# Performance work log

Measured on AMD Instinct MI355X. Metric: run time of the kernel, lower is better.

The kernel has to match this reference:

```python
import jax, jax.numpy as jnp
import numpy as np

BS = 512          # number of nodes (batch)
EMBED = 256       # embed_dim
NHEAD = 8
HDIM = EMBED // NHEAD
E = BS * BS       # fully-connected intra-batch graph


def _xavier(key, shape):
    lim = float(np.sqrt(6.0 / (shape[0] + shape[1])))
    return jax.random.uniform(key, shape, jnp.float32, -lim, lim)


def setup_inputs() -> dict:
    key = jax.random.key(0)
    ks = jax.random.split(key, 6)
    feats = jax.random.normal(ks[0], (BS, EMBED), jnp.float32)
    # edges sorted by destination c, exactly BS edges per destination
    dst = jnp.repeat(jnp.arange(BS), BS)   # c
    src = jnp.tile(jnp.arange(BS), BS)     # r
    edge_index = jnp.stack([src, dst], axis=1).astype(jnp.int32)  # [E, 2], cols (r, c)
    edge_attr = jnp.zeros((E, 1), jnp.float32)  # unused by forward
    return {
        "feats": feats,
        "edge_index": edge_index,
        "edge_attr": edge_attr,
        "Wq": _xavier(ks[1], (EMBED, EMBED)), "bq": jnp.zeros((EMBED,), jnp.float32),
        "Wk": _xavier(ks[2], (EMBED, EMBED)), "bk": jnp.zeros((EMBED,), jnp.float32),
        "Wv": _xavier(ks[3], (EMBED, EMBED)), "bv": jnp.zeros((EMBED,), jnp.float32),
        "Wo": _xavier(ks[4], (EMBED, EMBED)), "bo": jnp.zeros((EMBED,), jnp.float32),
    }


def reference(feats, edge_index, edge_attr, Wq, bq, Wk, bk, Wv, bv, Wo, bo):
    bs = feats.shape[0]
    scale = 1.0 / np.sqrt(HDIM)
    # QKV projections (torch Linear: x @ W.T + b), split heads -> [h, n, d]
    q = (feats @ Wq.T + bq).reshape(bs, NHEAD, HDIM).transpose(1, 0, 2)
    k = (feats @ Wk.T + bk).reshape(bs, NHEAD, HDIM).transpose(1, 0, 2)
    v = (feats @ Wv.T + bv).reshape(bs, NHEAD, HDIM).transpose(1, 0, 2)
    r, c = edge_index[:, 0], edge_index[:, 1]
    qe = q[:, c, :]   # [h, E, d] query of destination node
    ke = k[:, r, :]   # [h, E, d] key of source node
    ve = v[:, r, :]   # [h, E, d] value of source node
    sim = jnp.einsum('hed,hed->eh', qe, ke) * scale   # [E, h]
    # deterministic segment softmax over edges grouped by destination c
    m = jax.ops.segment_max(sim, c, num_segments=bs)  # [n, h]
    p = jnp.exp(sim - m[c])
    s = jax.ops.segment_sum(p, c, num_segments=bs)    # [n, h]
    attn = p / s[c]                                    # [E, h]
    # weight values and scatter-add per destination (aggr='add')
    out_e = attn.T[..., None] * ve                     # [h, E, d]
    out_e = out_e.transpose(1, 0, 2).reshape(-1, NHEAD * HDIM)  # [E, h*d]
    agg = jax.ops.segment_sum(out_e, c, num_segments=bs)        # [n, embed]
    return agg @ Wo.T + bo
```

## Files before the change

### kernel.cpp

```cpp
#include <hip/hip_runtime.h>

#define BS 512
#define EMBED 256
#define NHEAD 8
#define HDIM 32

typedef __attribute__((ext_vector_type(8))) short short8;
typedef __attribute__((ext_vector_type(4))) float f32x4;

__device__ inline f32x4 mfma16(short8 a, short8 b, f32x4 c) {
    return __builtin_amdgcn_mfma_f32_16x16x32_bf16(a, b, c, 0, 0, 0);
}

__device__ inline unsigned short f2bf(float x) {
    unsigned int u = __float_as_uint(x);
    u += 0x7FFFu + ((u >> 16) & 1u);
    return (unsigned short)(u >> 16);
}
__device__ inline float bf2f(unsigned short h) {
    return __uint_as_float(((unsigned int)h) << 16);
}
__device__ inline void split8(const float* p, short8& hi, short8& lo) {
    float4 a = *(const float4*)p;
    float4 b = *(const float4*)(p + 4);
    float x[8] = {a.x, a.y, a.z, a.w, b.x, b.y, b.z, b.w};
#pragma unroll
    for (int j = 0; j < 8; ++j) {
        unsigned short h = f2bf(x[j]);
        hi[j] = (short)h;
        lo[j] = (short)f2bf(x[j] - bf2f(h));
    }
}

__global__ __launch_bounds__(256) void qkv_fused(
    const float* __restrict__ feats,
    const float* __restrict__ Wq, const float* __restrict__ Wk,
    const float* __restrict__ Wv, const float* __restrict__ Wo,
    const float* __restrict__ bq, const float* __restrict__ bk,
    const float* __restrict__ bv,
    unsigned short* __restrict__ Qhi, unsigned short* __restrict__ Qlo,
    unsigned short* __restrict__ Khi, unsigned short* __restrict__ Klo,
    unsigned short* __restrict__ Vthi,
    unsigned short* __restrict__ Wohi, unsigned short* __restrict__ Wolo,
    float* __restrict__ OUT)
{
    const int gidx = blockIdx.x * 256 + threadIdx.x;

    for (int j = gidx; j < 32768; j += 24576) {
        float4 z = {0.f, 0.f, 0.f, 0.f};
        ((float4*)OUT)[j] = z;
    }
    for (int j = gidx; j < 16384; j += 24576) {
        float4 v = ((const float4*)Wo)[j];
        const int jrow = j >> 6;
        const int c4 = (j & 63) * 4;
        const int head = c4 >> 5, dim = c4 & 31;
        const int dst = head * (EMBED * HDIM) + jrow * HDIM + dim;
        ushort4 ph, pl;
        ph.x = f2bf(v.x); pl.x = f2bf(v.x - bf2f(ph.x));
        ph.y = f2bf(v.y); pl.y = f2bf(v.y - bf2f(ph.y));
        ph.z = f2bf(v.z); pl.z = f2bf(v.z - bf2f(ph.z));
        ph.w = f2bf(v.w); pl.w = f2bf(v.w - bf2f(ph.w));
        *(ushort4*)(Wohi + dst) = ph;
        *(ushort4*)(Wolo + dst) = pl;
    }

    const int wave = blockIdx.x * 4 + (threadIdx.x >> 6);
    const int l = threadIdx.x & 63;
    const int r = l & 15, g = l >> 4;
    const int nt = wave % 24, mt = wave / 24;
    const int m0 = mt * 32, n0 = nt * 32;
    const int seg = n0 >> 8;
    const int nn = n0 & 255;
    const float* W = (seg == 0) ? Wq : (seg == 1) ? Wk : Wv;
    const float* bias = (seg == 0) ? bq : (seg == 1) ? bk : bv;

    const float* a0 = feats + (m0 + r) * EMBED;
    const float* a1 = a0 + 16 * EMBED;
    const float* b0 = W + (nn + r) * EMBED;
    const float* b1 = b0 + 16 * EMBED;

    f32x4 acc00 = {0,0,0,0}, acc01 = {0,0,0,0}, acc10 = {0,0,0,0}, acc11 = {0,0,0,0};
#pragma unroll
    for (int kb = 0; kb < 8; ++kb) {
        const int k0 = kb * 32 + g * 8;
        short8 A0h, A0l, A1h, A1l, B0h, B0l, B1h, B1l;
        split8(a0 + k0, A0h, A0l);
        split8(a1 + k0, A1h, A1l);
        split8(b0 + k0, B0h, B0l);
        split8(b1 + k0, B1h, B1l);
        acc00 = mfma16(A0h, B0h, acc00);
        acc01 = mfma16(A0h, B1h, acc01);
        acc10 = mfma16(A1h, B0h, acc10);
        acc11 = mfma16(A1h, B1h, acc11);
        acc00 = mfma16(A0h, B0l, acc00);
        acc01 = mfma16(A0h, B1l, acc01);
        acc10 = mfma16(A1h, B0l, acc10);
        acc11 = mfma16(A1h, B1l, acc11);
        acc00 = mfma16(A0l, B0h, acc00);
        acc01 = mfma16(A0l, B1h, acc01);
        acc10 = mfma16(A1l, B0h, acc10);
        acc11 = mfma16(A1l, B1h, acc11);
    }

#pragma unroll
    for (int ti = 0; ti < 2; ++ti) {
#pragma unroll
        for (int tj = 0; tj < 2; ++tj) {
            f32x4 a = (ti == 0) ? (tj == 0 ? acc00 : acc01)
                                : (tj == 0 ? acc10 : acc11);
            const int cn = nn + tj * 16 + r;
            const float bb = bias[cn];
            if (seg < 2) {
                unsigned short* Dhi = seg ? Khi : Qhi;
                unsigned short* Dlo = seg ? Klo : Qlo;
                const int head = cn >> 5, dim = cn & 31;
#pragma unroll
                for (int r4 = 0; r4 < 4; ++r4) {
                    const int i = m0 + ti * 16 + g * 4 + r4;
                    float v = a[r4] + bb;
                    unsigned short hh = f2bf(v);
                    const int addr = head * (BS * HDIM) + i * HDIM + dim;
                    Dhi[addr] = hh;
                    Dlo[addr] = f2bf(v - bf2f(hh));
                }
            } else {
                const int i0 = m0 + ti * 16 + g * 4;
                ushort4 ph;
                ph.x = f2bf(a[0] + bb); ph.y = f2bf(a[1] + bb);
                ph.z = f2bf(a[2] + bb); ph.w = f2bf(a[3] + bb);
                *(ushort4*)(Vthi + cn * BS + i0) = ph;
            }
        }
    }
}

__global__ __launch_bounds__(512) void attn_out(
    const unsigned short* __restrict__ Qhi, const unsigned short* __restrict__ Qlo,
    const unsigned short* __restrict__ Khi, const unsigned short* __restrict__ Klo,
    const unsigned short* __restrict__ Vthi,
    const unsigned short* __restrict__ Wohi, const unsigned short* __restrict__ Wolo,
    const float* __restrict__ bo, float* __restrict__ OUT)
{
    const int qt = blockIdx.x >> 3;
    const int h = blockIdx.x & 7;
    const int q0 = qt * 16;
    const int tid = threadIdx.x;
    const int w = tid >> 6, l = tid & 63;
    const int r = l & 15, g = l >> 4;

    __shared__ unsigned short Psm[16 * 512];
    __shared__ float Opart[8][2][256];
    __shared__ float Rpart[8][16];
    __shared__ float Agg[16][36];
    char* Pb = (char*)Psm;

    const unsigned short* Kh = Khi + h * (BS * HDIM);
    const unsigned short* Kl = Klo + h * (BS * HDIM);
    const short8 qhi = *(const short8*)(Qhi + h * (BS * HDIM) + (q0 + r) * HDIM + g * 8);
    const short8 qlo = *(const short8*)(Qlo + h * (BS * HDIM) + (q0 + r) * HDIM + g * 8);

    const float cs = 0.17677669529663687f;
    float rs[4] = {0.f, 0.f, 0.f, 0.f};

#pragma unroll
    for (int kt = 0; kt < 4; ++kt) {
        const int krow = w * 64 + kt * 16 + r;
        short8 kh = *(const short8*)(Kh + krow * HDIM + g * 8);
        short8 kl = *(const short8*)(Kl + krow * HDIM + g * 8);
        f32x4 acc = {0.f, 0.f, 0.f, 0.f};
        acc = mfma16(qhi, kh, acc);
        acc = mfma16(qhi, kl, acc);
        acc = mfma16(qlo, kh, acc);
#pragma unroll
        for (int r4 = 0; r4 < 4; ++r4) {
            float p = __expf(acc[r4] * cs);
            rs[r4] += p;
            const int q = g * 4 + r4;
            const int bofs = q * 1024 + ((krow * 2) ^ ((q & 7) << 4));
            *(unsigned short*)(Pb + bofs) = f2bf(p);
        }
    }
#pragma unroll
    for (int off = 1; off < 16; off <<= 1) {
#pragma unroll
        for (int r4 = 0; r4 < 4; ++r4) rs[r4] += __shfl_xor(rs[r4], off);
    }
    if (r == 0) {
#pragma unroll
        for (int r4 = 0; r4 < 4; ++r4) Rpart[w][g * 4 + r4] = rs[r4];
    }

    f32x4 o0 = {0.f, 0.f, 0.f, 0.f}, o1 = {0.f, 0.f, 0.f, 0.f};
    const unsigned short* V0h = Vthi + (h * HDIM + r) * BS;
    const unsigned short* V1h = V0h + 16 * BS;
#pragma unroll
    for (int kc = 0; kc < 2; ++kc) {
        const int kb = w * 64 + kc * 32 + g * 8;
        const int bofs = r * 1024 + ((kb * 2) ^ ((r & 7) << 4));
        short8 pa = *(const short8*)(Pb + bofs);
        o0 = mfma16(pa, *(const short8*)(V0h + kb), o0);
        o1 = mfma16(pa, *(const short8*)(V1h + kb), o1);
    }
    ((f32x4*)&Opart[w][0][0])[l] = o0;
    ((f32x4*)&Opart[w][1][0])[l] = o1;
    __syncthreads();

    if (w < 2) {
        f32x4 o = ((f32x4*)&Opart[0][w][0])[l];
#pragma unroll
        for (int p = 1; p < 8; ++p) {
            f32x4 t = ((f32x4*)&Opart[p][w][0])[l];
            o[0] += t[0]; o[1] += t[1]; o[2] += t[2]; o[3] += t[3];
        }
#pragma unroll
        for (int r4 = 0; r4 < 4; ++r4) {
            const int q = g * 4 + r4;
            float rt = Rpart[0][q];
#pragma unroll
            for (int p = 1; p < 8; ++p) rt += Rpart[p][q];
            Agg[q][w * 16 + r] = o[r4] / rt;
        }
    }
    __syncthreads();

    short8 ah, al;
    split8(&Agg[r][g * 8], ah, al);
    const unsigned short* Woh = Wohi + h * (EMBED * HDIM);
    const unsigned short* Wol = Wolo + h * (EMBED * HDIM);
#pragma unroll
    for (int nsub = 0; nsub < 2; ++nsub) {
        const int j0 = w * 32 + nsub * 16;
        short8 bh = *(const short8*)(Woh + (j0 + r) * HDIM + g * 8);
        short8 bl = *(const short8*)(Wol + (j0 + r) * HDIM + g * 8);
        f32x4 a = {0.f, 0.f, 0.f, 0.f};
        a = mfma16(ah, bh, a);
        a = mfma16(ah, bl, a);
        a = mfma16(al, bh, a);
#pragma unroll
        for (int r4 = 0; r4 < 4; ++r4) {
            const int row = q0 + g * 4 + r4;
            const int col = j0 + r;
            float v = a[r4];
            if (h == 0) v += bo[col];
            atomicAdd(&OUT[row * EMBED + col], v);
        }
    }
}

extern "C" void kernel_launch(void* const* d_in, const int* in_sizes, int n_in,
                              void* d_out, int out_size, void* d_ws, size_t ws_size,
                              hipStream_t stream) {
    const float* feats = (const float*)d_in[0];
    const float* Wq = (const float*)d_in[3];
    const float* bq = (const float*)d_in[4];
    const float* Wk = (const float*)d_in[5];
    const float* bk = (const float*)d_in[6];
    const float* Wv = (const float*)d_in[7];
    const float* bv = (const float*)d_in[8];
    const float* Wo = (const float*)d_in[9];
    const float* bo = (const float*)d_in[10];
    float* out = (float*)d_out;

    unsigned short* ws = (unsigned short*)d_ws;
    const size_t NE = (size_t)BS * EMBED;
    const size_t WO = (size_t)EMBED * EMBED;
    unsigned short* Qhi  = ws;
    unsigned short* Qlo  = Qhi + NE;
    unsigned short* Khi  = Qlo + NE;
    unsigned short* Klo  = Khi + NE;
    unsigned short* Vthi = Klo + NE;
    unsigned short* Wohi = Vthi + NE;
    unsigned short* Wolo = Wohi + WO;

    qkv_fused<<<96, 256, 0, stream>>>(feats, Wq, Wk, Wv, Wo, bq, bk, bv,
                                      Qhi, Qlo, Khi, Klo, Vthi,
                                      Wohi, Wolo, out);
    attn_out<<<256, 512, 0, stream>>>(Qhi, Qlo, Khi, Klo, Vthi,
                                      Wohi, Wolo, bo, out);
}
```

Measured before the change: 24.86 us.

## Replace float atomics on output with per-head partials and last-block reduction

Each attention block now writes its per-head output-projection partial to a workspace buffer instead of issuing float atomicAdds into OUT. A per-query-tile counter picks the last of the 8 head blocks, which sums the partials, adds the bias and writes OUT with plain stores. This removes the need to zero OUT in the first kernel and removes contended atomics, giving a deterministic result. In exchange it adds a workspace round trip, a threadfence/counter step, and a serialized reduction tail in one block per tile.

After: 50.12 us. 102% more time.

```diff
diff --git a/kernel.cpp b/kernel.cpp
--- a/kernel.cpp
+++ b/kernel.cpp
@@ -42,14 +42,12 @@
     unsigned short* __restrict__ Khi, unsigned short* __restrict__ Klo,
     unsigned short* __restrict__ Vthi,
     unsigned short* __restrict__ Wohi, unsigned short* __restrict__ Wolo,
-    float* __restrict__ OUT)
+    int* __restrict__ cnt)
 {
     const int gidx = blockIdx.x * 256 + threadIdx.x;
 
-    for (int j = gidx; j < 32768; j += 24576) {
-        float4 z = {0.f, 0.f, 0.f, 0.f};
-        ((float4*)OUT)[j] = z;
-    }
+    if (gidx < 256) cnt[gidx] = 0;
+
     for (int j = gidx; j < 16384; j += 24576) {
         float4 v = ((const float4*)Wo)[j];
         const int jrow = j >> 6;
@@ -140,7 +138,8 @@
     const unsigned short* __restrict__ Khi, const unsigned short* __restrict__ Klo,
     const unsigned short* __restrict__ Vthi,
     const unsigned short* __restrict__ Wohi, const unsigned short* __restrict__ Wolo,
-    const float* __restrict__ bo, float* __restrict__ OUT)
+    const float* __restrict__ bo, float* __restrict__ parts,
+    int* __restrict__ cnt, float* __restrict__ OUT)
 {
     const int qt = blockIdx.x >> 3;
     const int h = blockIdx.x & 7;
@@ -153,6 +152,7 @@
     __shared__ float Opart[8][2][256];
     __shared__ float Rpart[8][16];
     __shared__ float Agg[16][36];
+    __shared__ int lastFlag;
     char* Pb = (char*)Psm;
 
     const unsigned short* Kh = Khi + h * (BS * HDIM);
@@ -224,6 +224,7 @@
     }
     __syncthreads();
 
+    float* Pp = parts + ((size_t)qt * NHEAD + h) * (16 * EMBED);
     short8 ah, al;
     split8(&Agg[r][g * 8], ah, al);
     const unsigned short* Woh = Wohi + h * (EMBED * HDIM);
@@ -239,11 +240,34 @@
         a = mfma16(al, bh, a);
 #pragma unroll
         for (int r4 = 0; r4 < 4; ++r4) {
-            const int row = q0 + g * 4 + r4;
-            const int col = j0 + r;
-            float v = a[r4];
-            if (h == 0) v += bo[col];
-            atomicAdd(&OUT[row * EMBED + col], v);
+            Pp[(g * 4 + r4) * EMBED + j0 + r] = a[r4];
+        }
+    }
+    __syncthreads();
+
+    if (tid == 0) {
+        __threadfence();
+        int old = atomicAdd(&cnt[qt], 1);
+        lastFlag = (old == NHEAD - 1) ? 1 : 0;
+    }
+    __syncthreads();
+
+    if (lastFlag) {
+        __threadfence();
+        const float* base = parts + (size_t)qt * NHEAD * (16 * EMBED);
+        const int c4 = (tid & 63) * 4;
+        const float4 bb = *(const float4*)(bo + c4);
+#pragma unroll
+        for (int half = 0; half < 2; ++half) {
+            const int q = (tid >> 6) + half * 8;
+            f32x4 s = {0.f, 0.f, 0.f, 0.f};
+#pragma unroll
+            for (int hh = 0; hh < NHEAD; ++hh) {
+                f32x4 t4 = *(const f32x4*)(base + hh * (16 * EMBED) + q * EMBED + c4);
+                s[0] += t4[0]; s[1] += t4[1]; s[2] += t4[2]; s[3] += t4[3];
+            }
+            float4 o = {s[0] + bb.x, s[1] + bb.y, s[2] + bb.z, s[3] + bb.w};
+            *(float4*)(OUT + (size_t)(q0 + q) * EMBED + c4) = o;
         }
     }
 }
@@ -272,10 +296,12 @@
     unsigned short* Vthi = Klo + NE;
     unsigned short* Wohi = Vthi + NE;
     unsigned short* Wolo = Wohi + WO;
+    float* parts = (float*)(Wolo + WO);
+    int* cnt = (int*)(parts + (size_t)32 * 8 * 16 * EMBED);
 
     qkv_fused<<<96, 256, 0, stream>>>(feats, Wq, Wk, Wv, Wo, bq, bk, bv,
                                       Qhi, Qlo, Khi, Klo, Vthi,
-                                      Wohi, Wolo, out);
+                                      Wohi, Wolo, cnt);
     attn_out<<<256, 512, 0, stream>>>(Qhi, Qlo, Khi, Klo, Vthi,
-                                      Wohi, Wolo, bo, out);
-}
+                                      Wohi, Wolo, bo, parts, cnt, out);
+}
```
